# Kernel optimization log

Measured on AMD Instinct MI355X. Metric: run time of the kernel, lower is better.

## Reference

```python
import jax, jax.numpy as jnp
import numpy as np

TOKENS, HIDDEN = 2048, 1024
N_EXPERTS, INTER, TOPK = 8, 2816, 2
RENORMALIZE = True


def setup_inputs() -> dict:
    key = jax.random.key(0)
    k1, k2, k3, k4 = jax.random.split(key, 4)
    x = jax.random.normal(k1, (TOKENS, HIDDEN), dtype=jnp.float32)
    gating_output = jax.random.normal(k2, (TOKENS, N_EXPERTS), dtype=jnp.float32)
    # stacked gate_proj+up_proj per expert: [E, 2*I, H]
    w1 = jax.random.normal(k3, (N_EXPERTS, 2 * INTER, HIDDEN), dtype=jnp.float32) * 0.02
    # down_proj per expert: [E, H, I]
    w2 = jax.random.normal(k4, (N_EXPERTS, HIDDEN, INTER), dtype=jnp.float32) * 0.02
    return {"x": x, "gating_output": gating_output, "w1": w1, "w2": w2}


def _moe(x, gating_output, w1, w2):
    # fused_topk: softmax over router logits, then top-k, then renormalize
    probs = jax.nn.softmax(gating_output, axis=-1)              # [T, E]
    topk_w, topk_ids = jax.lax.top_k(probs, TOPK)                # [T, K]
    if RENORMALIZE:
        topk_w = topk_w / jnp.sum(topk_w, axis=-1, keepdims=True)
    # fused_experts: gate/up proj -> SiLU(gate)*up -> down proj, per expert
    h = jnp.einsum('th,eih->tei', x, w1)                         # [T, E, 2I]
    gate, up = h[..., :INTER], h[..., INTER:]
    act = jax.nn.silu(gate) * up                                 # [T, E, I]
    out_e = jnp.einsum('tei,ehi->teh', act, w2)                  # [T, E, H]
    # combine: gather selected experts and weight them
    sel = jnp.take_along_axis(out_e, topk_ids[:, :, None], axis=1)  # [T, K, H]
    return jnp.sum(sel * topk_w[:, :, None].astype(sel.dtype), axis=1)  # [T, H]


def reference(x, gating_output, w1, w2):
    return _moe(x, gating_output, w1, w2)
```

## Files before the change

kernel.cpp:

```cpp
#include <hip/hip_runtime.h>
#include <hip/hip_bf16.h>

#define TOKENS 2048
#define HIDDEN 1024
#define NEXP   8
#define INTER  2816
#define N1     5632
#define ROWCAP 6144
#define MT     24
#define NT1    44
#define NT2    8
#define SPLITK 2

typedef __attribute__((ext_vector_type(8))) short short8;
typedef __attribute__((ext_vector_type(4))) float f32x4;

typedef unsigned int __attribute__((address_space(1))) as1_uint;
typedef unsigned int __attribute__((address_space(3))) as3_uint;

__device__ __forceinline__ void gload16(const void* g, void* l) {
  __builtin_amdgcn_global_load_lds((const as1_uint*)g, (as3_uint*)l, 16, 0, 0);
}

__device__ __forceinline__ unsigned short f2bf(float f) {
  unsigned u = __float_as_uint(f);
  u += 0x7fff + ((u >> 16) & 1);
  return (unsigned short)(u >> 16);
}
__device__ __forceinline__ float bf2f(unsigned short h) {
  return __uint_as_float(((unsigned)h) << 16);
}
__device__ __forceinline__ unsigned short bfs(float x) {
  __hip_bfloat16 h = __float2bfloat16(x);
  return *reinterpret_cast<unsigned short*>(&h);
}

__global__ void k_routing(const float* __restrict__ gate, int* __restrict__ ctrl,
                          int* __restrict__ tkid, float* __restrict__ tkw) {
  int t = blockIdx.x * blockDim.x + threadIdx.x;
  if (t >= TOKENS) return;
  float l[8];
#pragma unroll
  for (int i = 0; i < 8; i++) l[i] = gate[t * 8 + i];
  int i0 = 0; float m0 = l[0];
#pragma unroll
  for (int i = 1; i < 8; i++) if (l[i] > m0) { m0 = l[i]; i0 = i; }
  int i1 = -1; float m1 = -3.4e38f;
#pragma unroll
  for (int i = 0; i < 8; i++) if (i != i0 && l[i] > m1) { m1 = l[i]; i1 = i; }
  float e  = __expf(m1 - m0);
  float w0 = 1.f / (1.f + e);
  float w1 = e / (1.f + e);
  tkid[2 * t] = i0; tkid[2 * t + 1] = i1;
  tkw[2 * t] = w0;  tkw[2 * t + 1] = w1;
  atomicAdd(&ctrl[i0], 1);
  atomicAdd(&ctrl[i1], 1);
}

__global__ void k_base(int* ctrl) {
  if (threadIdx.x == 0) {
    int a = 0;
    for (int e = 0; e < 8; e++) { ctrl[16 + e] = a; a += ((ctrl[e] + 255) >> 8) << 8; }
  }
}

__global__ void k_fill(int* __restrict__ ctrl, const int* __restrict__ tkid,
                       int* __restrict__ rtok, int* __restrict__ trow) {
  int t = blockIdx.x * blockDim.x + threadIdx.x;
  if (t >= TOKENS) return;
#pragma unroll
  for (int k = 0; k < 2; k++) {
    int e = tkid[2 * t + k];
    int pos = atomicAdd(&ctrl[8 + e], 1);
    int row = ctrl[16 + e] + pos;
    rtok[row] = t;
    trow[2 * t + k] = row;
  }
}

__global__ void k_gather(const float* __restrict__ x, const int* __restrict__ ctrl,
                         const int* __restrict__ rtok, unsigned short* __restrict__ Abf) {
  int row = blockIdx.x;
  int e = -1, local = 0;
  for (int i = 0; i < 8; i++) {
    int b = ctrl[16 + i], p = ((ctrl[i] + 255) >> 8) << 8;
    if (row >= b && row < b + p) { e = i; local = row - b; break; }
  }
  if (e < 0) return;
  int tid = threadIdx.x;
  unsigned short* dst = Abf + (size_t)row * HIDDEN;
  if (local < ctrl[e]) {
    int t = rtok[row];
    float4 v = ((const float4*)(x + (size_t)t * HIDDEN))[tid];
    ushort4 o; o.x = f2bf(v.x); o.y = f2bf(v.y); o.z = f2bf(v.z); o.w = f2bf(v.w);
    ((ushort4*)dst)[tid] = o;
  } else {
    ushort4 z; z.x = 0; z.y = 0; z.z = 0; z.w = 0;
    ((ushort4*)dst)[tid] = z;
  }
}

__device__ __forceinline__ int tile_lookup(const int* ctrl, int mt, int* ml) {
  int a0 = 0;
  for (int i = 0; i < 8; i++) {
    int pt = (ctrl[i] + 255) >> 8;
    if (mt < a0 + pt) { *ml = mt - a0; return i; }
    a0 += pt;
  }
  return -1;
}

__global__ __launch_bounds__(512, 4) void k_gemm1(const float* __restrict__ w1,
    const unsigned short* __restrict__ Abf, unsigned short* __restrict__ act,
    const int* __restrict__ ctrl) {
  union __align__(16) LdsU {
    struct { unsigned char A[32768]; unsigned char Bf[32768]; unsigned char Bb[16384]; } st;
    unsigned short hb[256 * 132];
  };
  __shared__ LdsU lds;
  int bid = blockIdx.x;
  int wg = (bid & 7) * (NT1 * MT / 8) + (bid >> 3);
  int mt = wg / NT1, nt = wg % NT1;
  int ml; int e = tile_lookup(ctrl, mt, &ml);
  if (e < 0) return;
  int tid = threadIdx.x, lane = tid & 63, wid = tid >> 6, wr = wid >> 1, wc = wid & 1;
  int rbase = ctrl[16 + e] + ml * 256;
  const unsigned char* Ab = (const unsigned char*)(Abf + (size_t)rbase * HIDDEN);
  const unsigned char* Bw = (const unsigned char*)(w1 + (size_t)e * N1 * HIDDEN);
  int l3 = lane >> 3, l4 = lane >> 4, l15 = lane & 15;
  int swzA = ((lane & 7) ^ l3) << 4;

  size_t aoff[4], boff[4];
#pragma unroll
  for (int i = 0; i < 4; i++) {
    int g = wid * 4 + i;
    aoff[i] = (size_t)(g * 8 + l3) * (HIDDEN * 2) + swzA;
    int r = g * 4 + l4;
    int grow = (r < 64) ? nt * 64 + r : INTER + nt * 64 + (r - 64);
    boff[i] = (size_t)grow * (HIDDEN * 4) + (size_t)l15 * 16;
  }

  f32x4 acc[4][4];
  f32x4 zero = {0.f, 0.f, 0.f, 0.f};
#pragma unroll
  for (int i = 0; i < 4; i++)
#pragma unroll
    for (int j = 0; j < 4; j++) acc[i][j] = zero;

#pragma unroll
  for (int i = 0; i < 4; i++)
    gload16(Bw + boff[i], &lds.st.Bf[(wid * 4 + i) * 1024]);

  const int NS = HIDDEN / 64;
  for (int s = 0; s < NS; ++s) {
#pragma unroll
    for (int i = 0; i < 4; i++)
      gload16(Ab + aoff[i] + s * 128, &lds.st.A[(wid * 4 + i) * 1024]);
    __syncthreads();
#pragma unroll
    for (int i = 0; i < 4; i++) {
      int off = wid * 4096 + i * 1024 + lane * 16;
      f32x4 v = *(const f32x4*)&lds.st.Bf[off];
      int r = off >> 8, jL = (off >> 4) & 15;
      uint2 wv;
      wv.x = (unsigned)bfs(v[0]) | ((unsigned)bfs(v[1]) << 16);
      wv.y = (unsigned)bfs(v[2]) | ((unsigned)bfs(v[3]) << 16);
      *(uint2*)&lds.st.Bb[r * 128 + ((((jL >> 1) ^ (r & 7)) << 4) | ((jL & 1) << 3))] = wv;
    }
    __syncthreads();
    if (s + 1 < NS) {
#pragma unroll
      for (int i = 0; i < 4; i++)
        gload16(Bw + boff[i] + (size_t)(s + 1) * 256, &lds.st.Bf[(wid * 4 + i) * 1024]);
    }
#pragma unroll
    for (int ks = 0; ks < 2; ++ks) {
      short8 a[4], b[4];
#pragma unroll
      for (int mi = 0; mi < 4; mi++) {
        int row = wr * 64 + mi * 16 + l15;
        int koff = ks * 64 + (l4 << 4);
        a[mi] = *(const short8*)&lds.st.A[row * 128 + (koff ^ ((row & 7) << 4))];
      }
#pragma unroll
      for (int ni = 0; ni < 4; ni++) {
        int row = wc * 64 + ni * 16 + l15;
        int koff = ks * 64 + (l4 << 4);
        b[ni] = *(const short8*)&lds.st.Bb[row * 128 + (koff ^ ((row & 7) << 4))];
      }
#pragma unroll
      for (int mi = 0; mi < 4; mi++)
#pragma unroll
        for (int ni = 0; ni < 4; ni++)
          acc[mi][ni] = __builtin_amdgcn_mfma_f32_16x16x32_bf16(a[mi], b[ni], acc[mi][ni], 0, 0, 0);
    }
    __syncthreads();
  }
#pragma unroll
  for (int mi = 0; mi < 4; mi++)
#pragma unroll
    for (int ni = 0; ni < 4; ni++)
#pragma unroll
      for (int r = 0; r < 4; r++) {
        int row = wr * 64 + mi * 16 + (l4 << 2) + r;
        int col = wc * 64 + ni * 16 + l15;
        lds.hb[row * 132 + col] = f2bf(acc[mi][ni][r]);
      }
  __syncthreads();
  {
    int r = tid >> 1, ch = (tid & 1) * 32;
    unsigned short* orow = act + (size_t)(rbase + r) * INTER + nt * 64 + ch;
    const unsigned short* hrow = &lds.hb[r * 132];
#pragma unroll
    for (int j = 0; j < 32; j += 4) {
      ushort4 o;
#pragma unroll
      for (int q = 0; q < 4; q++) {
        float g = bf2f(hrow[ch + j + q]);
        float u = bf2f(hrow[64 + ch + j + q]);
        float s = g / (1.f + __expf(-g));
        ((unsigned short*)&o)[q] = f2bf(s * u);
      }
      *(ushort4*)(orow + j) = o;
    }
  }
}

__global__ __launch_bounds__(512, 4) void k_gemm2(const float* __restrict__ w2,
    const unsigned short* __restrict__ act, float* __restrict__ Pb,
    const int* __restrict__ ctrl) {
  struct __align__(16) Lds2 { unsigned char A[32768]; unsigned char Bf[32768]; unsigned char Bb[16384]; };
  __shared__ Lds2 lds;
  int bid = blockIdx.x;
  int wg = (bid & 7) * (NT2 * MT * SPLITK / 8) + (bid >> 3);
  int z = wg / (MT * NT2);
  int rem = wg % (MT * NT2);
  int mt = rem >> 3, nt = rem & 7;
  int ml; int e = tile_lookup(ctrl, mt, &ml);
  if (e < 0) return;
  int tid = threadIdx.x, lane = tid & 63, wid = tid >> 6, wr = wid >> 1, wc = wid & 1;
  int rbase = ctrl[16 + e] + ml * 256;
  const int KST = (INTER / 64) / SPLITK;
  const unsigned char* Ab = (const unsigned char*)(act + (size_t)rbase * INTER) + (size_t)z * KST * 128;
  const unsigned char* Bw = (const unsigned char*)(w2 + (size_t)e * HIDDEN * INTER) + (size_t)z * KST * 256;
  int l3 = lane >> 3, l4 = lane >> 4, l15 = lane & 15;
  int swzA = ((lane & 7) ^ l3) << 4;

  size_t aoff[4], boff[4];
#pragma unroll
  for (int i = 0; i < 4; i++) {
    int g = wid * 4 + i;
    aoff[i] = (size_t)(g * 8 + l3) * (INTER * 2) + swzA;
    int r = g * 4 + l4;
    boff[i] = (size_t)(nt * 128 + r) * (INTER * 4) + (size_t)l15 * 16;
  }

  f32x4 acc[4][4];
  f32x4 zero = {0.f, 0.f, 0.f, 0.f};
#pragma unroll
  for (int i = 0; i < 4; i++)
#pragma unroll
    for (int j = 0; j < 4; j++) acc[i][j] = zero;

#pragma unroll
  for (int i = 0; i < 4; i++)
    gload16(Bw + boff[i], &lds.Bf[(wid * 4 + i) * 1024]);

  for (int s = 0; s < KST; ++s) {
#pragma unroll
    for (int i = 0; i < 4; i++)
      gload16(Ab + aoff[i] + s * 128, &lds.A[(wid * 4 + i) * 1024]);
    __syncthreads();
#pragma unroll
    for (int i = 0; i < 4; i++) {
      int off = wid * 4096 + i * 1024 + lane * 16;
      f32x4 v = *(const f32x4*)&lds.Bf[off];
      int r = off >> 8, jL = (off >> 4) & 15;
      uint2 wv;
      wv.x = (unsigned)bfs(v[0]) | ((unsigned)bfs(v[1]) << 16);
      wv.y = (unsigned)bfs(v[2]) | ((unsigned)bfs(v[3]) << 16);
      *(uint2*)&lds.Bb[r * 128 + ((((jL >> 1) ^ (r & 7)) << 4) | ((jL & 1) << 3))] = wv;
    }
    __syncthreads();
    if (s + 1 < KST) {
#pragma unroll
      for (int i = 0; i < 4; i++)
        gload16(Bw + boff[i] + (size_t)(s + 1) * 256, &lds.Bf[(wid * 4 + i) * 1024]);
    }
#pragma unroll
    for (int ks = 0; ks < 2; ++ks) {
      short8 a[4], b[4];
#pragma unroll
      for (int mi = 0; mi < 4; mi++) {
        int row = wr * 64 + mi * 16 + l15;
        int koff = ks * 64 + (l4 << 4);
        a[mi] = *(const short8*)&lds.A[row * 128 + (koff ^ ((row & 7) << 4))];
      }
#pragma unroll
      for (int ni = 0; ni < 4; ni++) {
        int row = wc * 64 + ni * 16 + l15;
        int koff = ks * 64 + (l4 << 4);
        b[ni] = *(const short8*)&lds.Bb[row * 128 + (koff ^ ((row & 7) << 4))];
      }
#pragma unroll
      for (int mi = 0; mi < 4; mi++)
#pragma unroll
        for (int ni = 0; ni < 4; ni++)
          acc[mi][ni] = __builtin_amdgcn_mfma_f32_16x16x32_bf16(a[mi], b[ni], acc[mi][ni], 0, 0, 0);
    }
    __syncthreads();
  }
  float* P = Pb + (size_t)z * ROWCAP * HIDDEN;
#pragma unroll
  for (int mi = 0; mi < 4; mi++)
#pragma unroll
    for (int ni = 0; ni < 4; ni++) {
      int col = nt * 128 + wc * 64 + ni * 16 + l15;
#pragma unroll
      for (int r = 0; r < 4; r++) {
        int row = rbase + wr * 64 + mi * 16 + (l4 << 2) + r;
        P[(size_t)row * HIDDEN + col] = acc[mi][ni][r];
      }
    }
}

__global__ void k_finish(const float* __restrict__ Pb,
                         const int* __restrict__ trow, const float* __restrict__ tkw,
                         float* __restrict__ out) {
  int t = blockIdx.x, c = threadIdx.x;
  const float* P0 = Pb;
  const float* P1 = Pb + (size_t)ROWCAP * HIDDEN;
  int r0 = trow[2 * t], r1 = trow[2 * t + 1];
  float w0 = tkw[2 * t], w1 = tkw[2 * t + 1];
  float4 a0 = ((const float4*)(P0 + (size_t)r0 * HIDDEN))[c];
  float4 b0 = ((const float4*)(P1 + (size_t)r0 * HIDDEN))[c];
  float4 a1 = ((const float4*)(P0 + (size_t)r1 * HIDDEN))[c];
  float4 b1 = ((const float4*)(P1 + (size_t)r1 * HIDDEN))[c];
  float4 o;
  o.x = w0 * (a0.x + b0.x) + w1 * (a1.x + b1.x);
  o.y = w0 * (a0.y + b0.y) + w1 * (a1.y + b1.y);
  o.z = w0 * (a0.z + b0.z) + w1 * (a1.z + b1.z);
  o.w = w0 * (a0.w + b0.w) + w1 * (a1.w + b1.w);
  ((float4*)(out + (size_t)t * HIDDEN))[c] = o;
}

extern "C" void kernel_launch(void* const* d_in, const int* in_sizes, int n_in,
                              void* d_out, int out_size, void* d_ws, size_t ws_size,
                              hipStream_t stream) {
  const float* x      = (const float*)d_in[0];
  const float* gating = (const float*)d_in[1];
  const float* w1     = (const float*)d_in[2];
  const float* w2     = (const float*)d_in[3];
  float* out = (float*)d_out;
  char* ws = (char*)d_ws;

  int*   ctrl = (int*)ws;
  int*   tkid = (int*)(ws + 4096);
  float* tkw  = (float*)(ws + 24576);
  int*   rtok = (int*)(ws + 45056);
  int*   trow = (int*)(ws + 73728);
  size_t off_Abf = 131072;
  size_t off_act = off_Abf + (size_t)ROWCAP * HIDDEN * 2;
  size_t off_P   = off_act + (size_t)ROWCAP * INTER * 2;
  unsigned short* Abf  = (unsigned short*)(ws + off_Abf);
  unsigned short* actb = (unsigned short*)(ws + off_act);
  float* Pb = (float*)(ws + off_P);

  hipMemsetAsync(ws, 0, 1024, stream);

  k_routing<<<TOKENS / 256, 256, 0, stream>>>(gating, ctrl, tkid, tkw);
  k_base<<<1, 64, 0, stream>>>(ctrl);
  k_fill<<<TOKENS / 256, 256, 0, stream>>>(ctrl, tkid, rtok, trow);
  k_gather<<<ROWCAP, 256, 0, stream>>>(x, ctrl, rtok, Abf);
  k_gemm1<<<NT1 * MT, 512, 0, stream>>>(w1, Abf, actb, ctrl);
  k_gemm2<<<NT2 * MT * SPLITK, 512, 0, stream>>>(w2, actb, Pb, ctrl);
  k_finish<<<TOKENS, 256, 0, stream>>>(Pb, trow, tkw, out);
}
```

Baseline: 243.6 us.

## Shrink M tiles to 128 rows and convert fp32 weights to bf16 at fragment load

Expert row padding and GEMM M-tiles shrink from 256 to 128 rows, and workgroups drop to 256 threads, which cuts padding waste and gives more, smaller tiles. The separate pass that converted fp32 weights to bf16 in LDS, with its extra barrier, is removed. Weights are now read as fp32 from a swizzled LDS layout and packed to bf16 just before each MFMA. Tile order changes so consecutive blocks share a weight N-tile, which should help L2 reuse. In exchange, weights are re-read from global memory more times, conversion is repeated per wave, and the weight prefetch overlap is gone.

```diff
diff --git a/kernel.cpp b/kernel.cpp
--- a/kernel.cpp
+++ b/kernel.cpp
@@ -6,8 +6,8 @@
 #define NEXP   8
 #define INTER  2816
 #define N1     5632
-#define ROWCAP 6144
-#define MT     24
+#define ROWCAP 5120
+#define MT     40
 #define NT1    44
 #define NT2    8
 #define SPLITK 2
@@ -33,6 +33,12 @@
 __device__ __forceinline__ unsigned short bfs(float x) {
   __hip_bfloat16 h = __float2bfloat16(x);
   return *reinterpret_cast<unsigned short*>(&h);
+}
+__device__ __forceinline__ short8 pack8(f32x4 lo, f32x4 hi) {
+  short8 o;
+  o[0] = (short)bfs(lo[0]); o[1] = (short)bfs(lo[1]); o[2] = (short)bfs(lo[2]); o[3] = (short)bfs(lo[3]);
+  o[4] = (short)bfs(hi[0]); o[5] = (short)bfs(hi[1]); o[6] = (short)bfs(hi[2]); o[7] = (short)bfs(hi[3]);
+  return o;
 }
 
 __global__ void k_routing(const float* __restrict__ gate, int* __restrict__ ctrl,
@@ -60,7 +66,7 @@
 __global__ void k_base(int* ctrl) {
   if (threadIdx.x == 0) {
     int a = 0;
-    for (int e = 0; e < 8; e++) { ctrl[16 + e] = a; a += ((ctrl[e] + 255) >> 8) << 8; }
+    for (int e = 0; e < 8; e++) { ctrl[16 + e] = a; a += ((ctrl[e] + 127) >> 7) << 7; }
   }
 }
 
@@ -83,7 +89,7 @@
   int row = blockIdx.x;
   int e = -1, local = 0;
   for (int i = 0; i < 8; i++) {
-    int b = ctrl[16 + i], p = ((ctrl[i] + 255) >> 8) << 8;
+    int b = ctrl[16 + i], p = ((ctrl[i] + 127) >> 7) << 7;
     if (row >= b && row < b + p) { e = i; local = row - b; break; }
   }
   if (e < 0) return;
@@ -103,41 +109,44 @@
 __device__ __forceinline__ int tile_lookup(const int* ctrl, int mt, int* ml) {
   int a0 = 0;
   for (int i = 0; i < 8; i++) {
-    int pt = (ctrl[i] + 255) >> 8;
+    int pt = (ctrl[i] + 127) >> 7;
     if (mt < a0 + pt) { *ml = mt - a0; return i; }
     a0 += pt;
   }
   return -1;
 }
 
-__global__ __launch_bounds__(512, 4) void k_gemm1(const float* __restrict__ w1,
+__global__ __launch_bounds__(256, 3) void k_gemm1(const float* __restrict__ w1,
     const unsigned short* __restrict__ Abf, unsigned short* __restrict__ act,
     const int* __restrict__ ctrl) {
   union __align__(16) LdsU {
-    struct { unsigned char A[32768]; unsigned char Bf[32768]; unsigned char Bb[16384]; } st;
-    unsigned short hb[256 * 132];
+    struct { unsigned char A[16384]; unsigned char Bf[32768]; } st;
+    unsigned short hb[128 * 132];
   };
   __shared__ LdsU lds;
   int bid = blockIdx.x;
   int wg = (bid & 7) * (NT1 * MT / 8) + (bid >> 3);
-  int mt = wg / NT1, nt = wg % NT1;
+  int nt = wg / MT, mt = wg % MT;
   int ml; int e = tile_lookup(ctrl, mt, &ml);
   if (e < 0) return;
   int tid = threadIdx.x, lane = tid & 63, wid = tid >> 6, wr = wid >> 1, wc = wid & 1;
-  int rbase = ctrl[16 + e] + ml * 256;
+  int rbase = ctrl[16 + e] + ml * 128;
   const unsigned char* Ab = (const unsigned char*)(Abf + (size_t)rbase * HIDDEN);
   const unsigned char* Bw = (const unsigned char*)(w1 + (size_t)e * N1 * HIDDEN);
   int l3 = lane >> 3, l4 = lane >> 4, l15 = lane & 15;
   int swzA = ((lane & 7) ^ l3) << 4;
 
-  size_t aoff[4], boff[4];
+  unsigned aoff[4], boff[8];
 #pragma unroll
   for (int i = 0; i < 4; i++) {
     int g = wid * 4 + i;
-    aoff[i] = (size_t)(g * 8 + l3) * (HIDDEN * 2) + swzA;
-    int r = g * 4 + l4;
+    aoff[i] = (unsigned)(g * 8 + l3) * (HIDDEN * 2) + swzA;
+  }
+#pragma unroll
+  for (int i = 0; i < 8; i++) {
+    int r = (wid * 8 + i) * 4 + l4;
     int grow = (r < 64) ? nt * 64 + r : INTER + nt * 64 + (r - 64);
-    boff[i] = (size_t)grow * (HIDDEN * 4) + (size_t)l15 * 16;
+    boff[i] = (unsigned)grow * (HIDDEN * 4) + ((l15 ^ (r & 15)) << 4);
   }
 
   f32x4 acc[4][4];
@@ -147,32 +156,14 @@
 #pragma unroll
     for (int j = 0; j < 4; j++) acc[i][j] = zero;
 
-#pragma unroll
-  for (int i = 0; i < 4; i++)
-    gload16(Bw + boff[i], &lds.st.Bf[(wid * 4 + i) * 1024]);
-
-  const int NS = HIDDEN / 64;
-  for (int s = 0; s < NS; ++s) {
+  for (int kk = 0; kk < HIDDEN / 64; ++kk) {
 #pragma unroll
     for (int i = 0; i < 4; i++)
-      gload16(Ab + aoff[i] + s * 128, &lds.st.A[(wid * 4 + i) * 1024]);
+      gload16(Ab + (size_t)aoff[i] + kk * 128, &lds.st.A[(wid * 4 + i) * 1024]);
+#pragma unroll
+    for (int i = 0; i < 8; i++)
+      gload16(Bw + (size_t)boff[i] + kk * 256, &lds.st.Bf[(wid * 8 + i) * 1024]);
     __syncthreads();
-#pragma unroll
-    for (int i = 0; i < 4; i++) {
-      int off = wid * 4096 + i * 1024 + lane * 16;
-      f32x4 v = *(const f32x4*)&lds.st.Bf[off];
-      int r = off >> 8, jL = (off >> 4) & 15;
-      uint2 wv;
-      wv.x = (unsigned)bfs(v[0]) | ((unsigned)bfs(v[1]) << 16);
-      wv.y = (unsigned)bfs(v[2]) | ((unsigned)bfs(v[3]) << 16);
-      *(uint2*)&lds.st.Bb[r * 128 + ((((jL >> 1) ^ (r & 7)) << 4) | ((jL & 1) << 3))] = wv;
-    }
-    __syncthreads();
-    if (s + 1 < NS) {
-#pragma unroll
-      for (int i = 0; i < 4; i++)
-        gload16(Bw + boff[i] + (size_t)(s + 1) * 256, &lds.st.Bf[(wid * 4 + i) * 1024]);
-    }
 #pragma unroll
     for (int ks = 0; ks < 2; ++ks) {
       short8 a[4], b[4];
@@ -184,9 +175,11 @@
       }
 #pragma unroll
       for (int ni = 0; ni < 4; ni++) {
-        int row = wc * 64 + ni * 16 + l15;
-        int koff = ks * 64 + (l4 << 4);
-        b[ni] = *(const short8*)&lds.st.Bb[row * 128 + (koff ^ ((row & 7) << 4))];
+        int r = wc * 64 + ni * 16 + l15;
+        int c = ks * 8 + l4 * 2;
+        f32x4 lo = *(const f32x4*)&lds.st.Bf[r * 256 + ((c ^ (r & 15)) << 4)];
+        f32x4 hi = *(const f32x4*)&lds.st.Bf[r * 256 + (((c + 1) ^ (r & 15)) << 4)];
+        b[ni] = pack8(lo, hi);
       }
 #pragma unroll
       for (int mi = 0; mi < 4; mi++)
@@ -226,33 +219,36 @@
   }
 }
 
-__global__ __launch_bounds__(512, 4) void k_gemm2(const float* __restrict__ w2,
+__global__ __launch_bounds__(256, 3) void k_gemm2(const float* __restrict__ w2,
     const unsigned short* __restrict__ act, float* __restrict__ Pb,
     const int* __restrict__ ctrl) {
-  struct __align__(16) Lds2 { unsigned char A[32768]; unsigned char Bf[32768]; unsigned char Bb[16384]; };
+  struct __align__(16) Lds2 { unsigned char A[16384]; unsigned char Bf[32768]; };
   __shared__ Lds2 lds;
   int bid = blockIdx.x;
   int wg = (bid & 7) * (NT2 * MT * SPLITK / 8) + (bid >> 3);
-  int z = wg / (MT * NT2);
-  int rem = wg % (MT * NT2);
-  int mt = rem >> 3, nt = rem & 7;
+  int mt = wg % MT;
+  int p = wg / MT;
+  int z = p & 1, nt = p >> 1;
   int ml; int e = tile_lookup(ctrl, mt, &ml);
   if (e < 0) return;
   int tid = threadIdx.x, lane = tid & 63, wid = tid >> 6, wr = wid >> 1, wc = wid & 1;
-  int rbase = ctrl[16 + e] + ml * 256;
+  int rbase = ctrl[16 + e] + ml * 128;
   const int KST = (INTER / 64) / SPLITK;
   const unsigned char* Ab = (const unsigned char*)(act + (size_t)rbase * INTER) + (size_t)z * KST * 128;
   const unsigned char* Bw = (const unsigned char*)(w2 + (size_t)e * HIDDEN * INTER) + (size_t)z * KST * 256;
   int l3 = lane >> 3, l4 = lane >> 4, l15 = lane & 15;
   int swzA = ((lane & 7) ^ l3) << 4;
 
-  size_t aoff[4], boff[4];
+  unsigned aoff[4], boff[8];
 #pragma unroll
   for (int i = 0; i < 4; i++) {
     int g = wid * 4 + i;
-    aoff[i] = (size_t)(g * 8 + l3) * (INTER * 2) + swzA;
-    int r = g * 4 + l4;
-    boff[i] = (size_t)(nt * 128 + r) * (INTER * 4) + (size_t)l15 * 16;
+    aoff[i] = (unsigned)(g * 8 + l3) * (INTER * 2) + swzA;
+  }
+#pragma unroll
+  for (int i = 0; i < 8; i++) {
+    int r = (wid * 8 + i) * 4 + l4;
+    boff[i] = (unsigned)(nt * 128 + r) * (INTER * 4) + ((l15 ^ (r & 15)) << 4);
   }
 
   f32x4 acc[4][4];
@@ -262,31 +258,14 @@
 #pragma unroll
     for (int j = 0; j < 4; j++) acc[i][j] = zero;
 
-#pragma unroll
-  for (int i = 0; i < 4; i++)
-    gload16(Bw + boff[i], &lds.Bf[(wid * 4 + i) * 1024]);
-
   for (int s = 0; s < KST; ++s) {
 #pragma unroll
     for (int i = 0; i < 4; i++)
-      gload16(Ab + aoff[i] + s * 128, &lds.A[(wid * 4 + i) * 1024]);
+      gload16(Ab + (size_t)aoff[i] + s * 128, &lds.A[(wid * 4 + i) * 1024]);
+#pragma unroll
+    for (int i = 0; i < 8; i++)
+      gload16(Bw + (size_t)boff[i] + s * 256, &lds.Bf[(wid * 8 + i) * 1024]);
     __syncthreads();
-#pragma unroll
-    for (int i = 0; i < 4; i++) {
-      int off = wid * 4096 + i * 1024 + lane * 16;
-      f32x4 v = *(const f32x4*)&lds.Bf[off];
-      int r = off >> 8, jL = (off >> 4) & 15;
-      uint2 wv;
-      wv.x = (unsigned)bfs(v[0]) | ((unsigned)bfs(v[1]) << 16);
-      wv.y = (unsigned)bfs(v[2]) | ((unsigned)bfs(v[3]) << 16);
-      *(uint2*)&lds.Bb[r * 128 + ((((jL >> 1) ^ (r & 7)) << 4) | ((jL & 1) << 3))] = wv;
-    }
-    __syncthreads();
-    if (s + 1 < KST) {
-#pragma unroll
-      for (int i = 0; i < 4; i++)
-        gload16(Bw + boff[i] + (size_t)(s + 1) * 256, &lds.Bf[(wid * 4 + i) * 1024]);
-    }
 #pragma unroll
     for (int ks = 0; ks < 2; ++ks) {
       short8 a[4], b[4];
@@ -298,9 +277,11 @@
       }
 #pragma unroll
       for (int ni = 0; ni < 4; ni++) {
-        int row = wc * 64 + ni * 16 + l15;
-        int koff = ks * 64 + (l4 << 4);
-        b[ni] = *(const short8*)&lds.Bb[row * 128 + (koff ^ ((row & 7) << 4))];
+        int r = wc * 64 + ni * 16 + l15;
+        int c = ks * 8 + l4 * 2;
+        f32x4 lo = *(const f32x4*)&lds.Bf[r * 256 + ((c ^ (r & 15)) << 4)];
+        f32x4 hi = *(const f32x4*)&lds.Bf[r * 256 + (((c + 1) ^ (r & 15)) << 4)];
+        b[ni] = pack8(lo, hi);
       }
 #pragma unroll
       for (int mi = 0; mi < 4; mi++)
@@ -372,7 +353,7 @@
   k_base<<<1, 64, 0, stream>>>(ctrl);
   k_fill<<<TOKENS / 256, 256, 0, stream>>>(ctrl, tkid, rtok, trow);
   k_gather<<<ROWCAP, 256, 0, stream>>>(x, ctrl, rtok, Abf);
-  k_gemm1<<<NT1 * MT, 512, 0, stream>>>(w1, Abf, actb, ctrl);
-  k_gemm2<<<NT2 * MT * SPLITK, 512, 0, stream>>>(w2, actb, Pb, ctrl);
+  k_gemm1<<<NT1 * MT, 256, 0, stream>>>(w1, Abf, actb, ctrl);
+  k_gemm2<<<NT2 * MT * SPLITK, 256, 0, stream>>>(w2, actb, Pb, ctrl);
   k_finish<<<TOKENS, 256, 0, stream>>>(Pb, trow, tkw, out);
 }
```

After: 239.2 us. About the same (-1.8%).
